# Performance work log

Hardware: AMD Instinct MI355X
Metric: run time of the kernel (lower is better)

## Reference

```python
import jax, jax.numpy as jnp
import numpy as np

V = 50000; C0 = 2000; C1 = 10000   # vocab and adaptive-softmax cutoffs
E = 512; H = 1024; B = 32; T = 128
H1 = H // 4; H2 = H // 16           # div_val = 4.0 per source formula
S1 = C1 - C0; S2 = V - C1


def setup_inputs() -> dict:
    key = jax.random.key(0)
    ks = jax.random.split(key, 12)
    # lengths sorted descending, max length == T (required by output.view(b*(T-1),-1))
    lengths = jnp.sort(jax.random.randint(ks[0], (B,), T // 2, T + 1))[::-1]
    lengths = lengths.at[0].set(T).astype(jnp.int64)
    x = jax.random.randint(ks[1], (B, T), 1, V)
    x = jnp.where(jnp.arange(T)[None, :] < lengths[:, None], x, 0).astype(jnp.int64)  # PAD=0 beyond length
    emb = (jax.random.normal(ks[2], (V, E), jnp.float32) * 0.02).at[0].set(0.0)  # padding_idx=0
    w_ih = jax.random.normal(ks[3], (3 * H, E), jnp.float32) * 0.02
    w_hh = jax.random.normal(ks[4], (3 * H, H), jnp.float32) * 0.02
    b_ih = jnp.zeros((3 * H,), jnp.float32)
    b_hh = jnp.zeros((3 * H,), jnp.float32)
    head_w = jax.random.normal(ks[5], (C0 + 2, H), jnp.float32) * 0.02   # shortlist + 2 cluster logits
    p1 = jax.random.normal(ks[6], (H1, H), jnp.float32) * 0.02
    t1 = jax.random.normal(ks[7], (S1, H1), jnp.float32) * 0.02
    p2 = jax.random.normal(ks[8], (H2, H), jnp.float32) * 0.02
    t2 = jax.random.normal(ks[9], (S2, H2), jnp.float32) * 0.02
    hidden = jnp.zeros((1, B, H), jnp.float32)
    return dict(x=x, lengths=lengths, hidden=hidden, emb=emb, w_ih=w_ih, w_hh=w_hh,
                b_ih=b_ih, b_hh=b_hh, head_w=head_w, p1=p1, t1=t1, p2=p2, t2=t2)


def gru_masked(inp, h0, w_ih, w_hh, b_ih, b_hh, lengths):
    """Torch GRU on packed sequence of lengths-1: frozen hidden + zero outputs past length."""
    xp = jnp.einsum('bte,ge->btg', inp, w_ih) + b_ih  # [B, T-1, 3H] input projections

    def step(h, args):
        xpt, t = args
        hp = h @ w_hh.T + b_hh
        xr, xz, xn = jnp.split(xpt, 3, axis=-1)
        hr, hz, hn = jnp.split(hp, 3, axis=-1)
        r = jax.nn.sigmoid(xr + hr)
        z = jax.nn.sigmoid(xz + hz)
        n = jnp.tanh(xn + r * hn)
        h_new = (1.0 - z) * n + z * h
        valid = (t < lengths - 1)[:, None]
        h = jnp.where(valid, h_new, h)          # freeze hidden past sequence end
        y = jnp.where(valid, h, 0.0)            # pad_packed_sequence zero-fills
        return h, y

    steps = jnp.arange(inp.shape[1])
    hT, ys = jax.lax.scan(step, h0, (jnp.swapaxes(xp, 0, 1), steps))
    return jnp.swapaxes(ys, 0, 1), hT  # [B, T-1, H], [B, H]


def adaptive_loss(out, targets, head_w, p1, t1, p2, t2):
    """AdaptiveLogSoftmaxWithLoss: mean NLL over shortlist + 2 tail clusters."""
    N = out.shape[0]
    head_lp = jax.nn.log_softmax(out @ head_w.T, axis=-1)  # [N, C0+2]
    idx = jnp.arange(N)
    lp_short = head_lp[idx, jnp.clip(targets, 0, C0 - 1)]

    def cluster_lp(p, t, ci, lo, size):
        tail_lp = jax.nn.log_softmax((out @ p.T) @ t.T, axis=-1)  # [N, size]
        rel = jnp.clip(targets - lo, 0, size - 1)
        return head_lp[:, C0 + ci] + tail_lp[idx, rel]

    lp1 = cluster_lp(p1, t1, 0, C0, S1)
    lp2 = cluster_lp(p2, t2, 1, C1, S2)
    logp = jnp.where(targets < C0, lp_short, jnp.where(targets < C1, lp1, lp2))
    return -jnp.mean(logp)


def reference(x, lengths, hidden, emb, w_ih, w_hh, b_ih, b_hh, head_w, p1, t1, p2, t2):
    inp = emb[x][:, :T - 1]  # dropout=0.0 -> identity
    ys, hT = gru_masked(inp, hidden[0], w_ih, w_hh, b_ih, b_hh, lengths)
    out = ys.reshape(B * (T - 1), H)
    targets = x[:, 1:].reshape(-1)
    loss = adaptive_loss(out, targets, head_w, p1, t1, p2, t2)
    return loss, hT[None]
```

## Files before the change

### kernel.cpp

```cpp
#include <hip/hip_runtime.h>
#include <math.h>

#define VV   50000
#define CC0  2000
#define CC1  10000
#define ED   512
#define HD   1024
#define BBATCH 32
#define TT   128
#define HH1  256
#define HH2  64
#define SS1  8000
#define SS2  40000
#define NR   4064
#define G3   3072

#define OFF_XP   0ull
#define OFF_YSB  12484608ull
#define OFF_HB   14565376ull
#define OFF_HT   14598144ull
#define OFF_P1B  14630912ull
#define OFF_P2B  15151104ull
#define OFF_WHB  15281152ull
#define OFF_T1B  16306176ull
#define OFF_PP1  17330176ull
#define OFF_PP2  17461248ull
#define OFF_SUM  17494016ull
#define OFF_LOSS (OFF_SUM + 6ull*4064ull)
#define OFF_INT  (OFF_LOSS + 64ull)
#define OFF_WIHB (OFF_INT + 8ull*4064ull)

#define ZERO_N (6*4064 + 64)
#define NBG 64

typedef __attribute__((ext_vector_type(8))) __bf16 bf16x8;
typedef __attribute__((ext_vector_type(4))) float f32x4;
typedef __attribute__((ext_vector_type(4))) unsigned int u32x4;
typedef unsigned long long u64;
typedef unsigned short u16;
struct ull2s { u64 x, y; };

__device__ __forceinline__ u16 f2bf(float f) {
    unsigned u = __builtin_bit_cast(unsigned, f);
    u += 0x7fff + ((u >> 16) & 1);
    return (u16)(u >> 16);
}

__global__ void init_k(const float* __restrict__ hidden, u16* __restrict__ hb0,
                       float* __restrict__ zreg, int* __restrict__ cnt1,
                       int* __restrict__ cnt2, int* __restrict__ bar)
{
    int i = blockIdx.x * 256 + threadIdx.x;
    if (i < BBATCH * HD) hb0[i] = f2bf(hidden[i]);
    int zi = i - BBATCH * HD;
    if (zi >= 0 && zi < ZERO_N) zreg[zi] = 0.f;
    if (zi == ZERO_N) { *cnt1 = 0; *cnt2 = 0; }
    int bi = zi - (ZERO_N + 1);
    if (bi >= 0 && bi < 2048) bar[bi] = 0;
}

__global__ void prep_k(const int* __restrict__ x, int* __restrict__ targets,
                       int* __restrict__ hselc, int* __restrict__ list1,
                       int* __restrict__ list2, int* __restrict__ cnt1, int* __restrict__ cnt2)
{
    int n = blockIdx.x * 256 + threadIdx.x;
    if (n >= NR) return;
    int b = n / 127, t = n % 127;
    int tgt = x[b * TT + t + 1];
    targets[n] = tgt;
    hselc[n] = (tgt < CC0) ? tgt : ((tgt < CC1) ? CC0 : CC0 + 1);
    if (tgt >= CC0 && tgt < CC1) list1[atomicAdd(cnt1, 1)] = n;
    else if (tgt >= CC1)         list2[atomicAdd(cnt2, 1)] = n;
}

__global__ void cvt_bf16_k(const float* __restrict__ src, u16* __restrict__ dst, int n4)
{
    int i = blockIdx.x * 256 + threadIdx.x;
    if (i >= n4) return;
    float4 f = *(const float4*)(src + 4 * (size_t)i);
    union { u16 h[4]; u64 v; } u;
    u.h[0] = f2bf(f.x); u.h[1] = f2bf(f.y); u.h[2] = f2bf(f.z); u.h[3] = f2bf(f.w);
    *(u64*)&dst[4 * (size_t)i] = u.v;
}

__global__ void cvt_multi_k(const float* __restrict__ s0, u16* __restrict__ d0, int n0,
                            const float* __restrict__ s1, u16* __restrict__ d1, int n1,
                            const float* __restrict__ s2, u16* __restrict__ d2, int n2,
                            const float* __restrict__ s3, u16* __restrict__ d3, int n3,
                            const float* __restrict__ s4, u16* __restrict__ d4, int n4)
{
    int i = blockIdx.x * 256 + threadIdx.x;
    const float* s; u16* d; int off = i;
    if (off < n0) { s = s0; d = d0; }
    else if ((off -= n0) < n1) { s = s1; d = d1; }
    else if ((off -= n1) < n2) { s = s2; d = d2; }
    else if ((off -= n2) < n3) { s = s3; d = d3; }
    else if ((off -= n3) < n4) { s = s4; d = d4; }
    else return;
    float4 f = *(const float4*)(s + 4 * (size_t)off);
    union { u16 h[4]; u64 v; } u;
    u.h[0] = f2bf(f.x); u.h[1] = f2bf(f.y); u.h[2] = f2bf(f.z); u.h[3] = f2bf(f.w);
    *(u64*)&d[4 * (size_t)off] = u.v;
}

__global__ void emb_gather_k(const int* __restrict__ x, const float* __restrict__ emb,
                             u16* __restrict__ embA)
{
    int idx = blockIdx.x * 256 + threadIdx.x;
    if (idx >= NR * 64) return;
    int n = idx >> 6;
    int kk = (idx & 63) << 3;
    int b = n & 31, t = n >> 5;
    int tok = x[b * TT + t];
    const float* ap = emb + (size_t)tok * ED + kk;
    float4 f0 = *(const float4*)ap;
    float4 f1 = *(const float4*)(ap + 4);
    union { u16 h[8]; u32x4 v; } u;
    u.h[0] = f2bf(f0.x); u.h[1] = f2bf(f0.y); u.h[2] = f2bf(f0.z); u.h[3] = f2bf(f0.w);
    u.h[4] = f2bf(f1.x); u.h[5] = f2bf(f1.y); u.h[6] = f2bf(f1.z); u.h[7] = f2bf(f1.w);
    *(u32x4*)&embA[(size_t)n * ED + kk] = u.v;
}

template<int EPI, int BFP32>
__global__ void __launch_bounds__(256)
mfma_gemm_k(const u16* __restrict__ Ab, const void* __restrict__ Bsrc,
            int Mdirect, int N, int K,
            const int* __restrict__ rowmap, const int* __restrict__ cntp,
            u16* __restrict__ outB, int ldo,
            float* __restrict__ gsum, float* __restrict__ gsel,
            const int* __restrict__ selcol, const int* __restrict__ targets, int lo)
{
    const int M = cntp ? *cntp : Mdirect;
    const int rbase = blockIdx.x * 128;
    if (rbase >= M) return;
    const int cbase = blockIdx.y * 128;

    __shared__ u16 As[128 * 40];
    __shared__ u16 Bs[128 * 40];
    __shared__ const u16* aptr[128];
    __shared__ int rown[128];
    __shared__ float redl[128 * 2];

    const int tid = threadIdx.x;
    if (tid < 128) {
        int rid = -1;
        if (rbase + tid < M) rid = rowmap ? rowmap[rbase + tid] : (rbase + tid);
        rown[tid] = rid;
        aptr[tid] = (rid >= 0) ? (Ab + (size_t)rid * K) : nullptr;
    }
    __syncthreads();

    const int lane = tid & 63, wid = tid >> 6;
    const int n16 = lane & 15, quad = lane >> 4;
    const int m0 = (wid >> 1) * 64, n0 = (wid & 1) * 64;
    const int i = tid >> 1, half = tid & 1;

    f32x4 acc[4][4];
#pragma unroll
    for (int a = 0; a < 4; a++)
#pragma unroll
        for (int b = 0; b < 4; b++) acc[a][b] = (f32x4){0.f, 0.f, 0.f, 0.f};

    for (int k0 = 0; k0 < K; k0 += 32) {
        const u16* ap = aptr[i];
        u32x4 a0 = {0,0,0,0}, a1 = a0;
        if (ap) {
            a0 = *(const u32x4*)(ap + k0 + half * 16);
            a1 = *(const u32x4*)(ap + k0 + half * 16 + 8);
        }
        u32x4 b0 = {0,0,0,0}, b1 = b0;
        int c = cbase + i;
        if (c < N) {
            if (BFP32) {
                const float* bp = (const float*)Bsrc + (size_t)c * K + k0 + half * 16;
                float4 f0 = *(const float4*)(bp);
                float4 f1 = *(const float4*)(bp + 4);
                float4 f2 = *(const float4*)(bp + 8);
                float4 f3 = *(const float4*)(bp + 12);
                union { u16 h[16]; u32x4 v[2]; } u;
                u.h[0]=f2bf(f0.x); u.h[1]=f2bf(f0.y); u.h[2]=f2bf(f0.z); u.h[3]=f2bf(f0.w);
                u.h[4]=f2bf(f1.x); u.h[5]=f2bf(f1.y); u.h[6]=f2bf(f1.z); u.h[7]=f2bf(f1.w);
                u.h[8]=f2bf(f2.x); u.h[9]=f2bf(f2.y); u.h[10]=f2bf(f2.z); u.h[11]=f2bf(f2.w);
                u.h[12]=f2bf(f3.x); u.h[13]=f2bf(f3.y); u.h[14]=f2bf(f3.z); u.h[15]=f2bf(f3.w);
                b0 = u.v[0]; b1 = u.v[1];
            } else {
                const u16* bp = (const u16*)Bsrc + (size_t)c * K + k0 + half * 16;
                b0 = *(const u32x4*)(bp);
                b1 = *(const u32x4*)(bp + 8);
            }
        }
        __syncthreads();
        *(u32x4*)&As[i * 40 + half * 16]     = a0;
        *(u32x4*)&As[i * 40 + half * 16 + 8] = a1;
        *(u32x4*)&Bs[i * 40 + half * 16]     = b0;
        *(u32x4*)&Bs[i * 40 + half * 16 + 8] = b1;
        __syncthreads();

        bf16x8 av[4], bv[4];
#pragma unroll
        for (int mi = 0; mi < 4; mi++)
            av[mi] = *(const bf16x8*)&As[(m0 + mi * 16 + n16) * 40 + quad * 8];
#pragma unroll
        for (int ni = 0; ni < 4; ni++)
            bv[ni] = *(const bf16x8*)&Bs[(n0 + ni * 16 + n16) * 40 + quad * 8];
#pragma unroll
        for (int mi = 0; mi < 4; mi++)
#pragma unroll
            for (int ni = 0; ni < 4; ni++)
                acc[mi][ni] = __builtin_amdgcn_mfma_f32_16x16x32_bf16(
                    av[mi], bv[ni], acc[mi][ni], 0, 0, 0);
    }

    __syncthreads();
    if (EPI == 0) {
#pragma unroll
        for (int mi = 0; mi < 4; mi++)
#pragma unroll
            for (int ni = 0; ni < 4; ni++)
#pragma unroll
                for (int r = 0; r < 4; r++) {
                    int row = rbase + m0 + mi * 16 + quad * 4 + r;
                    int col = cbase + n0 + ni * 16 + n16;
                    if (row < M && col < N)
                        outB[(size_t)row * ldo + col] = f2bf(acc[mi][ni][r]);
                }
    } else if (EPI == 3) {
#pragma unroll
        for (int mi = 0; mi < 4; mi++)
#pragma unroll
            for (int ni = 0; ni < 4; ni++)
#pragma unroll
                for (int r = 0; r < 4; r++) {
                    int row = rbase + m0 + mi * 16 + quad * 4 + r;
                    int col = cbase + n0 + ni * 16 + n16;
                    if (row < M && col < N)
                        gsum[(size_t)row * ldo + col] = acc[mi][ni][r] + gsel[col];
                }
    } else {
#pragma unroll
        for (int mi = 0; mi < 4; mi++)
#pragma unroll
            for (int r = 0; r < 4; r++) {
                int lrow = m0 + mi * 16 + quad * 4 + r;
                int nid = rown[lrow];
                float s = 0.f;
                if (nid >= 0) {
                    int sc = (EPI == 1) ? selcol[nid] : (targets[nid] - lo);
#pragma unroll
                    for (int ni = 0; ni < 4; ni++) {
                        int col = cbase + n0 + ni * 16 + n16;
                        if (col < N) {
                            float v = acc[mi][ni][r];
                            s += __expf(v);
                            if (col == sc) gsel[nid] = v;
                        }
                    }
                }
                s += __shfl_xor(s, 1);
                s += __shfl_xor(s, 2);
                s += __shfl_xor(s, 4);
                s += __shfl_xor(s, 8);
                if (n16 == 0) redl[lrow * 2 + (wid & 1)] = s;
            }
        __syncthreads();
        if (tid < 128) {
            int nid = rown[tid];
            if (nid >= 0) atomicAdd(&gsum[nid], redl[tid * 2] + redl[tid * 2 + 1]);
        }
    }
}

__global__ void __launch_bounds__(128, 1)
gru_persist_k(const float* __restrict__ xp, const float* __restrict__ hidden,
              u16* __restrict__ hb0, u16* __restrict__ hb1,
              const float* __restrict__ w_hh, const float* __restrict__ b_hh,
              const int* __restrict__ lengths, u16* __restrict__ ys,
              float* __restrict__ hT, int* __restrict__ cntbar)
{
    __shared__ u16 Blds[48 * 1032];
    const int tid = threadIdx.x;
    const int bid = blockIdx.x;
    const int j0 = bid * 16;
    const int lane = tid & 63, wid = tid >> 6;
    const int n16 = lane & 15, quad = lane >> 4;

    for (int idx = tid; idx < 48 * 1024; idx += 128) {
        int r = idx >> 10, k = idx & 1023;
        int g = r >> 4, c = r & 15;
        Blds[r * 1032 + k] = f2bf(w_hh[(size_t)(g * HD + j0 + c) * HD + k]);
    }

    const int col = j0 + n16;
    float bh0 = b_hh[col], bh1 = b_hh[HD + col], bh2 = b_hh[2 * HD + col];
    float hold[4];
    int len[4];
#pragma unroll
    for (int r = 0; r < 4; r++) {
        int b = wid * 16 + quad * 4 + r;
        len[r] = lengths[b];
        hold[r] = hidden[b * HD + col];
    }
    __syncthreads();

    float xrv[4], xzv[4], xnv[4];
#pragma unroll
    for (int r = 0; r < 4; r++) {
        int b = wid * 16 + quad * 4 + r;
        const float* xpt = xp + (size_t)b * G3 + col;
        xrv[r] = xpt[0]; xzv[r] = xpt[HD]; xnv[r] = xpt[2 * HD];
    }

    for (int t = 0; t < TT - 1; t++) {
        if (t > 0) {
            const int target = NBG * t;
            int guard = 0;
            while (__hip_atomic_load(cntbar, __ATOMIC_RELAXED,
                                     __HIP_MEMORY_SCOPE_AGENT) < target
                   && guard < (1 << 20)) {
                __builtin_amdgcn_s_sleep(1);
                guard++;
            }
        }
        asm volatile("" ::: "memory");

        const u16* hb = (t & 1) ? hb1 : hb0;
        u16* hbn = (t & 1) ? hb0 : hb1;

        const u16* arow = hb + (size_t)(wid * 16 + n16) * HD + quad * 8;
        u64 apf[64];
#pragma unroll
        for (int ks = 0; ks < 32; ks++) {
            apf[2*ks]   = __hip_atomic_load((const u64*)(arow + ks*32),
                                            __ATOMIC_RELAXED, __HIP_MEMORY_SCOPE_AGENT);
            apf[2*ks+1] = __hip_atomic_load((const u64*)(arow + ks*32 + 4),
                                            __ATOMIC_RELAXED, __HIP_MEMORY_SCOPE_AGENT);
        }

        f32x4 acc0 = {0.f, 0.f, 0.f, 0.f}, acc1 = acc0, acc2 = acc0;
        const int boff = n16 * 1032 + quad * 8;
#pragma unroll
        for (int ks = 0; ks < 32; ks++) {
            ull2s av2; av2.x = apf[2*ks]; av2.y = apf[2*ks+1];
            bf16x8 av = __builtin_bit_cast(bf16x8, av2);
            bf16x8 b0 = *(const bf16x8*)&Blds[boff + ks*32];
            bf16x8 b1 = *(const bf16x8*)&Blds[16*1032 + boff + ks*32];
            bf16x8 b2 = *(const bf16x8*)&Blds[32*1032 + boff + ks*32];
            acc0 = __builtin_amdgcn_mfma_f32_16x16x32_bf16(av, b0, acc0, 0, 0, 0);
            acc1 = __builtin_amdgcn_mfma_f32_16x16x32_bf16(av, b1, acc1, 0, 0, 0);
            acc2 = __builtin_amdgcn_mfma_f32_16x16x32_bf16(av, b2, acc2, 0, 0, 0);
        }

        float ysv[4];
#pragma unroll
        for (int r = 0; r < 4; r++) {
            int b = wid * 16 + quad * 4 + r;
            float hr = acc0[r] + bh0, hz = acc1[r] + bh1, hn = acc2[r] + bh2;
            float rg = 1.f / (1.f + __expf(-(xrv[r] + hr)));
            float zg = 1.f / (1.f + __expf(-(xzv[r] + hz)));
            float nv = tanhf(xnv[r] + rg * hn);
            bool valid = t < (len[r] - 1);
            float hnew = valid ? (1.f - zg) * nv + zg * hold[r] : hold[r];
            hold[r] = hnew;
            ysv[r] = valid ? hnew : 0.f;
            __hip_atomic_store(hbn + (size_t)b * HD + col, f2bf(hnew),
                               __ATOMIC_RELAXED, __HIP_MEMORY_SCOPE_AGENT);
        }

        __builtin_amdgcn_s_waitcnt(0);
        __syncthreads();
        if (tid == 0)
            __hip_atomic_fetch_add(cntbar, 1, __ATOMIC_RELAXED,
                                   __HIP_MEMORY_SCOPE_AGENT);

#pragma unroll
        for (int r = 0; r < 4; r++) {
            int b = wid * 16 + quad * 4 + r;
            ys[((size_t)b * 127 + t) * HD + col] = f2bf(ysv[r]);
            if (t == TT - 2) hT[b * HD + col] = hold[r];
        }
        const int tn = (t < TT - 2) ? t + 1 : t;
#pragma unroll
        for (int r = 0; r < 4; r++) {
            int b = wid * 16 + quad * 4 + r;
            const float* xpt = xp + ((size_t)tn * BBATCH + b) * G3 + col;
            xrv[r] = xpt[0]; xzv[r] = xpt[HD]; xnv[r] = xpt[2 * HD];
        }
    }
}

__global__ void finish_k(const float* __restrict__ hsum, const float* __restrict__ hsel,
                         const float* __restrict__ t1sum, const float* __restrict__ t1sel,
                         const float* __restrict__ t2sum, const float* __restrict__ t2sel,
                         const int* __restrict__ targets, float* __restrict__ losssum)
{
    __shared__ float red[256];
    int n = blockIdx.x * 256 + threadIdx.x;
    float lp = 0.f;
    if (n < NR) {
        lp = hsel[n] - logf(hsum[n]);
        int tgt = targets[n];
        if (tgt >= CC1)      lp += t2sel[n] - logf(t2sum[n]);
        else if (tgt >= CC0) lp += t1sel[n] - logf(t1sum[n]);
    }
    red[threadIdx.x] = lp;
    __syncthreads();
    for (int s = 128; s > 0; s >>= 1) {
        if (threadIdx.x < s) red[threadIdx.x] += red[threadIdx.x + s];
        __syncthreads();
    }
    if (threadIdx.x == 0) atomicAdd(losssum, red[0]);
}

__global__ void out_k(const float* __restrict__ losssum, const float* __restrict__ hT,
                      float* __restrict__ out)
{
    int i = blockIdx.x * 256 + threadIdx.x;
    if (i == 0) out[0] = -losssum[0] / (float)NR;
    if (i < BBATCH * HD) out[1 + i] = hT[i];
}

extern "C" void kernel_launch(void* const* d_in, const int* in_sizes, int n_in,
                              void* d_out, int out_size, void* d_ws, size_t ws_size,
                              hipStream_t stream)
{
    const int*   x       = (const int*)d_in[0];
    const int*   lengths = (const int*)d_in[1];
    const float* hidden  = (const float*)d_in[2];
    const float* emb     = (const float*)d_in[3];
    const float* w_ih    = (const float*)d_in[4];
    const float* w_hh    = (const float*)d_in[5];
    const float* b_ih    = (const float*)d_in[6];
    const float* b_hh    = (const float*)d_in[7];
    const float* head_w  = (const float*)d_in[8];
    const float* p1      = (const float*)d_in[9];
    const float* t1      = (const float*)d_in[10];
    const float* p2      = (const float*)d_in[11];
    const float* t2      = (const float*)d_in[12];

    float* ws = (float*)d_ws;
    float* xp    = ws + OFF_XP;
    u16*   ysb   = (u16*)(ws + OFF_YSB);
    u16*   hb0   = (u16*)(ws + OFF_HB);
    u16*   hb1   = hb0 + BBATCH * HD;
    float* hT    = ws + OFF_HT;
    u16*   p1b   = (u16*)(ws + OFF_P1B);
    u16*   p2b   = (u16*)(ws + OFF_P2B);
    u16*   whb   = (u16*)(ws + OFF_WHB);
    u16*   t1b   = (u16*)(ws + OFF_T1B);
    u16*   pp1b  = (u16*)(ws + OFF_PP1);
    u16*   pp2b  = (u16*)(ws + OFF_PP2);
    float* hsum  = ws + OFF_SUM;
    float* hsel  = hsum + 4064;
    float* t1sum = hsel + 4064;
    float* t1sel = t1sum + 4064;
    float* t2sum = t1sel + 4064;
    float* t2sel = t2sum + 4064;
    float* losss = ws + OFF_LOSS;
    int* ib      = (int*)(ws + OFF_INT);
    int* targets = ib;
    int* hselc   = ib + 4064;
    int* list1   = ib + 2 * 4064;
    int* list2   = ib + 3 * 4064;
    int* cnt1    = ib + 4 * 4064;
    int* cnt2    = cnt1 + 1;
    int* bar     = ib + 5 * 4064;

    u16* embA = (u16*)(ws + OFF_YSB);
    u16* wihb = (u16*)(ws + OFF_WIHB);
    u16* t2b  = (u16*)(ws + OFF_XP);

    float* out = (float*)d_out;

    init_k<<<232, 256, 0, stream>>>(hidden, hb0, hsum, cnt1, cnt2, bar);
    prep_k<<<16, 256, 0, stream>>>(x, targets, hselc, list1, list2, cnt1, cnt2);

    cvt_multi_k<<<(1499648 + 255) / 256, 256, 0, stream>>>(
        w_ih, wihb, 393216,
        head_w, whb, 512512,
        t1, t1b, 512000,
        p1, pp1b, 65536,
        p2, pp2b, 16384);

    emb_gather_k<<<(NR * 64 + 255) / 256, 256, 0, stream>>>(x, emb, embA);
    mfma_gemm_k<3, 0><<<dim3(32, 24), 256, 0, stream>>>(
        embA, wihb, NR, G3, ED, nullptr, nullptr, nullptr, G3,
        xp, (float*)b_ih, nullptr, nullptr, 0);

    gru_persist_k<<<NBG, 128, 0, stream>>>(xp, hidden, hb0, hb1, w_hh, b_hh,
                                           lengths, ysb, hT, bar);

    cvt_bf16_k<<<(640000 + 255) / 256, 256, 0, stream>>>(t2, t2b, 640000);

    mfma_gemm_k<0, 0><<<dim3(32, 2), 256, 0, stream>>>(
        ysb, pp1b, NR, HH1, HD, nullptr, nullptr, p1b, HH1,
        nullptr, nullptr, nullptr, nullptr, 0);
    mfma_gemm_k<0, 0><<<dim3(32, 1), 256, 0, stream>>>(
        ysb, pp2b, NR, HH2, HD, nullptr, nullptr, p2b, HH2,
        nullptr, nullptr, nullptr, nullptr, 0);
    mfma_gemm_k<1, 0><<<dim3(32, 16), 256, 0, stream>>>(
        ysb, whb, NR, CC0 + 2, HD, nullptr, nullptr, nullptr, 0,
        hsum, hsel, hselc, nullptr, 0);
    mfma_gemm_k<2, 0><<<dim3(32, 63), 256, 0, stream>>>(
        p1b, t1b, 0, SS1, HH1, list1, cnt1, nullptr, 0,
        t1sum, t1sel, nullptr, targets, CC0);
    mfma_gemm_k<2, 0><<<dim3(32, 313), 256, 0, stream>>>(
        p2b, t2b, 0, SS2, HH2, list2, cnt2, nullptr, 0,
        t2sum, t2sel, nullptr, targets, CC1);

    finish_k<<<16, 256, 0, stream>>>(hsum, hsel, t1sum, t1sel, t2sum, t2sel,
                                     targets, losss);
    out_k<<<128, 256, 0, stream>>>(losss, hT, out);
}
```

Measured before the change: 1.463 ms.

## Replace GRU grid counter barrier with per-block flags and triple-buffered hidden state

```diff
diff --git a/kernel.cpp b/kernel.cpp
--- a/kernel.cpp
+++ b/kernel.cpp
@@ -272,10 +272,10 @@
 
 __global__ void __launch_bounds__(128, 1)
 gru_persist_k(const float* __restrict__ xp, const float* __restrict__ hidden,
-              u16* __restrict__ hb0, u16* __restrict__ hb1,
+              u16* __restrict__ hb0, u16* __restrict__ hb1, u16* __restrict__ hb2,
               const float* __restrict__ w_hh, const float* __restrict__ b_hh,
               const int* __restrict__ lengths, u16* __restrict__ ys,
-              float* __restrict__ hT, int* __restrict__ cntbar)
+              float* __restrict__ hT, int* __restrict__ flags)
 {
     __shared__ u16 Blds[48 * 1032];
     const int tid = threadIdx.x;
@@ -310,44 +310,61 @@
         xrv[r] = xpt[0]; xzv[r] = xpt[HD]; xnv[r] = xpt[2 * HD];
     }
 
+    const int boff = n16 * 1032 + quad * 8;
+    const size_t rowoff = (size_t)(wid * 16 + n16) * HD + quad * 8;
+
     for (int t = 0; t < TT - 1; t++) {
-        if (t > 0) {
-            const int target = NBG * t;
-            int guard = 0;
-            while (__hip_atomic_load(cntbar, __ATOMIC_RELAXED,
-                                     __HIP_MEMORY_SCOPE_AGENT) < target
-                   && guard < (1 << 20)) {
-                __builtin_amdgcn_s_sleep(1);
-                guard++;
+        int m3 = t % 3;
+        const u16* hbR = (m3 == 0) ? hb0 : ((m3 == 1) ? hb1 : hb2);
+        int w3 = (t + 1) % 3;
+        u16* hbW = (w3 == 0) ? hb0 : ((w3 == 1) ? hb1 : hb2);
+
+        f32x4 acc0 = {0.f, 0.f, 0.f, 0.f}, acc1 = acc0, acc2 = acc0;
+
+        unsigned rem = 0xFFFFFFFFu;
+        int spin = 0;
+        while (rem) {
+            int f = __hip_atomic_load(&flags[lane * 32], __ATOMIC_RELAXED,
+                                      __HIP_MEMORY_SCOPE_AGENT);
+            u64 m = __ballot(f >= t);
+            u64 q = m & (m >> 1);
+            unsigned ready = 0;
+#pragma unroll
+            for (int ks = 0; ks < 32; ks++)
+                ready |= (unsigned)((q >> (2 * ks)) & 1ull) << ks;
+            unsigned todo = ready & rem;
+            if (!todo) {
+                if (++spin < (1 << 18)) { __builtin_amdgcn_s_sleep(2); continue; }
+                todo = rem;
             }
-        }
-        asm volatile("" ::: "memory");
-
-        const u16* hb = (t & 1) ? hb1 : hb0;
-        u16* hbn = (t & 1) ? hb0 : hb1;
-
-        const u16* arow = hb + (size_t)(wid * 16 + n16) * HD + quad * 8;
-        u64 apf[64];
-#pragma unroll
-        for (int ks = 0; ks < 32; ks++) {
-            apf[2*ks]   = __hip_atomic_load((const u64*)(arow + ks*32),
-                                            __ATOMIC_RELAXED, __HIP_MEMORY_SCOPE_AGENT);
-            apf[2*ks+1] = __hip_atomic_load((const u64*)(arow + ks*32 + 4),
-                                            __ATOMIC_RELAXED, __HIP_MEMORY_SCOPE_AGENT);
-        }
-
-        f32x4 acc0 = {0.f, 0.f, 0.f, 0.f}, acc1 = acc0, acc2 = acc0;
-        const int boff = n16 * 1032 + quad * 8;
-#pragma unroll
-        for (int ks = 0; ks < 32; ks++) {
-            ull2s av2; av2.x = apf[2*ks]; av2.y = apf[2*ks+1];
-            bf16x8 av = __builtin_bit_cast(bf16x8, av2);
-            bf16x8 b0 = *(const bf16x8*)&Blds[boff + ks*32];
-            bf16x8 b1 = *(const bf16x8*)&Blds[16*1032 + boff + ks*32];
-            bf16x8 b2 = *(const bf16x8*)&Blds[32*1032 + boff + ks*32];
-            acc0 = __builtin_amdgcn_mfma_f32_16x16x32_bf16(av, b0, acc0, 0, 0, 0);
-            acc1 = __builtin_amdgcn_mfma_f32_16x16x32_bf16(av, b1, acc1, 0, 0, 0);
-            acc2 = __builtin_amdgcn_mfma_f32_16x16x32_bf16(av, b2, acc2, 0, 0, 0);
+            todo = __builtin_amdgcn_readfirstlane(todo);
+            {
+                u64 a0buf[32], a1buf[32];
+#pragma unroll
+                for (int ks = 0; ks < 32; ks++) {
+                    if (todo & (1u << ks)) {
+                        const u16* ap = hbR + rowoff + ks * 32;
+                        a0buf[ks] = __hip_atomic_load((const u64*)ap,
+                                        __ATOMIC_RELAXED, __HIP_MEMORY_SCOPE_AGENT);
+                        a1buf[ks] = __hip_atomic_load((const u64*)(ap + 4),
+                                        __ATOMIC_RELAXED, __HIP_MEMORY_SCOPE_AGENT);
+                    }
+                }
+#pragma unroll
+                for (int ks = 0; ks < 32; ks++) {
+                    if (todo & (1u << ks)) {
+                        ull2s av2; av2.x = a0buf[ks]; av2.y = a1buf[ks];
+                        bf16x8 av = __builtin_bit_cast(bf16x8, av2);
+                        bf16x8 b0 = *(const bf16x8*)&Blds[boff + ks * 32];
+                        bf16x8 b1 = *(const bf16x8*)&Blds[16 * 1032 + boff + ks * 32];
+                        bf16x8 b2 = *(const bf16x8*)&Blds[32 * 1032 + boff + ks * 32];
+                        acc0 = __builtin_amdgcn_mfma_f32_16x16x32_bf16(av, b0, acc0, 0, 0, 0);
+                        acc1 = __builtin_amdgcn_mfma_f32_16x16x32_bf16(av, b1, acc1, 0, 0, 0);
+                        acc2 = __builtin_amdgcn_mfma_f32_16x16x32_bf16(av, b2, acc2, 0, 0, 0);
+                    }
+                }
+            }
+            rem &= ~todo;
         }
 
         float ysv[4];
@@ -362,15 +379,15 @@
             float hnew = valid ? (1.f - zg) * nv + zg * hold[r] : hold[r];
             hold[r] = hnew;
             ysv[r] = valid ? hnew : 0.f;
-            __hip_atomic_store(hbn + (size_t)b * HD + col, f2bf(hnew),
+            __hip_atomic_store(hbW + (size_t)b * HD + col, f2bf(hnew),
                                __ATOMIC_RELAXED, __HIP_MEMORY_SCOPE_AGENT);
         }
 
         __builtin_amdgcn_s_waitcnt(0);
         __syncthreads();
         if (tid == 0)
-            __hip_atomic_fetch_add(cntbar, 1, __ATOMIC_RELAXED,
-                                   __HIP_MEMORY_SCOPE_AGENT);
+            __hip_atomic_store(&flags[bid * 32], t + 1, __ATOMIC_RELAXED,
+                               __HIP_MEMORY_SCOPE_AGENT);
 
 #pragma unroll
         for (int r = 0; r < 4; r++) {
@@ -463,15 +480,16 @@
     int* list2   = ib + 3 * 4064;
     int* cnt1    = ib + 4 * 4064;
     int* cnt2    = cnt1 + 1;
-    int* bar     = ib + 5 * 4064;
+    int* flags   = ib + 5 * 4064;
 
     u16* embA = (u16*)(ws + OFF_YSB);
     u16* wihb = (u16*)(ws + OFF_WIHB);
     u16* t2b  = (u16*)(ws + OFF_XP);
+    u16* hb2  = (u16*)(ws + OFF_P1B);
 
     float* out = (float*)d_out;
 
-    init_k<<<232, 256, 0, stream>>>(hidden, hb0, hsum, cnt1, cnt2, bar);
+    init_k<<<232, 256, 0, stream>>>(hidden, hb0, hsum, cnt1, cnt2, flags);
     prep_k<<<16, 256, 0, stream>>>(x, targets, hselc, list1, list2, cnt1, cnt2);
 
     cvt_multi_k<<<(1499648 + 255) / 256, 256, 0, stream>>>(
@@ -486,8 +504,8 @@
         embA, wihb, NR, G3, ED, nullptr, nullptr, nullptr, G3,
         xp, (float*)b_ih, nullptr, nullptr, 0);
 
-    gru_persist_k<<<NBG, 128, 0, stream>>>(xp, hidden, hb0, hb1, w_hh, b_hh,
-                                           lengths, ysb, hT, bar);
+    gru_persist_k<<<NBG, 128, 0, stream>>>(xp, hidden, hb0, hb1, hb2, w_hh, b_hh,
+                                           lengths, ysb, hT, flags);
 
     cvt_bf16_k<<<(640000 + 255) / 256, 256, 0, stream>>>(t2, t2b, 640000);
 
```

Result: slower. 1.785 ms (+22.0%).

## Replace global counter barrier with per-block flags and partial early MFMA

Applied to the files above, without the earlier changes.

```diff
diff --git a/kernel.cpp b/kernel.cpp
--- a/kernel.cpp
+++ b/kernel.cpp
@@ -275,7 +275,7 @@
               u16* __restrict__ hb0, u16* __restrict__ hb1,
               const float* __restrict__ w_hh, const float* __restrict__ b_hh,
               const int* __restrict__ lengths, u16* __restrict__ ys,
-              float* __restrict__ hT, int* __restrict__ cntbar)
+              float* __restrict__ hT, int* __restrict__ flags)
 {
     __shared__ u16 Blds[48 * 1032];
     const int tid = threadIdx.x;
@@ -310,44 +310,107 @@
         xrv[r] = xpt[0]; xzv[r] = xpt[HD]; xnv[r] = xpt[2 * HD];
     }
 
+    const int boff = n16 * 1032 + quad * 8;
+    const size_t rowoff = (size_t)(wid * 16 + n16) * HD + quad * 8;
+
     for (int t = 0; t < TT - 1; t++) {
-        if (t > 0) {
-            const int target = NBG * t;
+        const u16* hbR = (t & 1) ? hb1 : hb0;
+        u16* hbW = (t & 1) ? hb0 : hb1;
+
+        f32x4 acc0 = {0.f, 0.f, 0.f, 0.f}, acc1 = acc0, acc2 = acc0;
+        u64 apf[64];
+
+        int fl = __hip_atomic_load(&flags[lane * 32], __ATOMIC_RELAXED,
+                                   __HIP_MEMORY_SCOPE_AGENT);
+        u64 rdy = __ballot(fl >= t);
+        unsigned done = 0;
+
+        if (rdy != ~0ull) {
+            u64 q = rdy & (rdy >> 1);
+            unsigned r0 = 0;
+#pragma unroll
+            for (int ks = 0; ks < 32; ks++)
+                r0 |= (unsigned)((q >> (2 * ks)) & 1ull) << ks;
+            r0 = __builtin_amdgcn_readfirstlane(r0);
+            asm volatile("" ::: "memory");
+            if (r0) {
+#pragma unroll
+                for (int ks = 0; ks < 32; ks++)
+                    if (r0 & (1u << ks)) {
+                        const u16* ap = hbR + rowoff + ks * 32;
+                        apf[2*ks]   = __hip_atomic_load((const u64*)ap,
+                                          __ATOMIC_RELAXED, __HIP_MEMORY_SCOPE_AGENT);
+                        apf[2*ks+1] = __hip_atomic_load((const u64*)(ap + 4),
+                                          __ATOMIC_RELAXED, __HIP_MEMORY_SCOPE_AGENT);
+                    }
+#pragma unroll
+                for (int ks = 0; ks < 32; ks++)
+                    if (r0 & (1u << ks)) {
+                        ull2s av2; av2.x = apf[2*ks]; av2.y = apf[2*ks+1];
+                        bf16x8 av = __builtin_bit_cast(bf16x8, av2);
+                        bf16x8 b0 = *(const bf16x8*)&Blds[boff + ks*32];
+                        bf16x8 b1 = *(const bf16x8*)&Blds[16*1032 + boff + ks*32];
+                        bf16x8 b2 = *(const bf16x8*)&Blds[32*1032 + boff + ks*32];
+                        acc0 = __builtin_amdgcn_mfma_f32_16x16x32_bf16(av, b0, acc0, 0, 0, 0);
+                        acc1 = __builtin_amdgcn_mfma_f32_16x16x32_bf16(av, b1, acc1, 0, 0, 0);
+                        acc2 = __builtin_amdgcn_mfma_f32_16x16x32_bf16(av, b2, acc2, 0, 0, 0);
+                    }
+                done = r0;
+            }
             int guard = 0;
-            while (__hip_atomic_load(cntbar, __ATOMIC_RELAXED,
-                                     __HIP_MEMORY_SCOPE_AGENT) < target
-                   && guard < (1 << 20)) {
+            while (true) {
+                fl = __hip_atomic_load(&flags[lane * 32], __ATOMIC_RELAXED,
+                                       __HIP_MEMORY_SCOPE_AGENT);
+                if (__ballot(fl >= t) == ~0ull) break;
+                if (++guard >= (1 << 20)) break;
                 __builtin_amdgcn_s_sleep(1);
-                guard++;
             }
         }
         asm volatile("" ::: "memory");
 
-        const u16* hb = (t & 1) ? hb1 : hb0;
-        u16* hbn = (t & 1) ? hb0 : hb1;
-
-        const u16* arow = hb + (size_t)(wid * 16 + n16) * HD + quad * 8;
-        u64 apf[64];
-#pragma unroll
-        for (int ks = 0; ks < 32; ks++) {
-            apf[2*ks]   = __hip_atomic_load((const u64*)(arow + ks*32),
-                                            __ATOMIC_RELAXED, __HIP_MEMORY_SCOPE_AGENT);
-            apf[2*ks+1] = __hip_atomic_load((const u64*)(arow + ks*32 + 4),
-                                            __ATOMIC_RELAXED, __HIP_MEMORY_SCOPE_AGENT);
-        }
-
-        f32x4 acc0 = {0.f, 0.f, 0.f, 0.f}, acc1 = acc0, acc2 = acc0;
-        const int boff = n16 * 1032 + quad * 8;
-#pragma unroll
-        for (int ks = 0; ks < 32; ks++) {
-            ull2s av2; av2.x = apf[2*ks]; av2.y = apf[2*ks+1];
-            bf16x8 av = __builtin_bit_cast(bf16x8, av2);
-            bf16x8 b0 = *(const bf16x8*)&Blds[boff + ks*32];
-            bf16x8 b1 = *(const bf16x8*)&Blds[16*1032 + boff + ks*32];
-            bf16x8 b2 = *(const bf16x8*)&Blds[32*1032 + boff + ks*32];
-            acc0 = __builtin_amdgcn_mfma_f32_16x16x32_bf16(av, b0, acc0, 0, 0, 0);
-            acc1 = __builtin_amdgcn_mfma_f32_16x16x32_bf16(av, b1, acc1, 0, 0, 0);
-            acc2 = __builtin_amdgcn_mfma_f32_16x16x32_bf16(av, b2, acc2, 0, 0, 0);
+        if (done == 0u) {
+#pragma unroll
+            for (int ks = 0; ks < 32; ks++) {
+                const u16* ap = hbR + rowoff + ks * 32;
+                apf[2*ks]   = __hip_atomic_load((const u64*)ap,
+                                  __ATOMIC_RELAXED, __HIP_MEMORY_SCOPE_AGENT);
+                apf[2*ks+1] = __hip_atomic_load((const u64*)(ap + 4),
+                                  __ATOMIC_RELAXED, __HIP_MEMORY_SCOPE_AGENT);
+            }
+#pragma unroll
+            for (int ks = 0; ks < 32; ks++) {
+                ull2s av2; av2.x = apf[2*ks]; av2.y = apf[2*ks+1];
+                bf16x8 av = __builtin_bit_cast(bf16x8, av2);
+                bf16x8 b0 = *(const bf16x8*)&Blds[boff + ks*32];
+                bf16x8 b1 = *(const bf16x8*)&Blds[16*1032 + boff + ks*32];
+                bf16x8 b2 = *(const bf16x8*)&Blds[32*1032 + boff + ks*32];
+                acc0 = __builtin_amdgcn_mfma_f32_16x16x32_bf16(av, b0, acc0, 0, 0, 0);
+                acc1 = __builtin_amdgcn_mfma_f32_16x16x32_bf16(av, b1, acc1, 0, 0, 0);
+                acc2 = __builtin_amdgcn_mfma_f32_16x16x32_bf16(av, b2, acc2, 0, 0, 0);
+            }
+        } else {
+            unsigned rem = ~done;
+#pragma unroll
+            for (int ks = 0; ks < 32; ks++)
+                if (rem & (1u << ks)) {
+                    const u16* ap = hbR + rowoff + ks * 32;
+                    apf[2*ks]   = __hip_atomic_load((const u64*)ap,
+                                      __ATOMIC_RELAXED, __HIP_MEMORY_SCOPE_AGENT);
+                    apf[2*ks+1] = __hip_atomic_load((const u64*)(ap + 4),
+                                      __ATOMIC_RELAXED, __HIP_MEMORY_SCOPE_AGENT);
+                }
+#pragma unroll
+            for (int ks = 0; ks < 32; ks++)
+                if (rem & (1u << ks)) {
+                    ull2s av2; av2.x = apf[2*ks]; av2.y = apf[2*ks+1];
+                    bf16x8 av = __builtin_bit_cast(bf16x8, av2);
+                    bf16x8 b0 = *(const bf16x8*)&Blds[boff + ks*32];
+                    bf16x8 b1 = *(const bf16x8*)&Blds[16*1032 + boff + ks*32];
+                    bf16x8 b2 = *(const bf16x8*)&Blds[32*1032 + boff + ks*32];
+                    acc0 = __builtin_amdgcn_mfma_f32_16x16x32_bf16(av, b0, acc0, 0, 0, 0);
+                    acc1 = __builtin_amdgcn_mfma_f32_16x16x32_bf16(av, b1, acc1, 0, 0, 0);
+                    acc2 = __builtin_amdgcn_mfma_f32_16x16x32_bf16(av, b2, acc2, 0, 0, 0);
+                }
         }
 
         float ysv[4];
@@ -362,15 +425,15 @@
             float hnew = valid ? (1.f - zg) * nv + zg * hold[r] : hold[r];
             hold[r] = hnew;
             ysv[r] = valid ? hnew : 0.f;
-            __hip_atomic_store(hbn + (size_t)b * HD + col, f2bf(hnew),
+            __hip_atomic_store(hbW + (size_t)b * HD + col, f2bf(hnew),
                                __ATOMIC_RELAXED, __HIP_MEMORY_SCOPE_AGENT);
         }
 
         __builtin_amdgcn_s_waitcnt(0);
         __syncthreads();
         if (tid == 0)
-            __hip_atomic_fetch_add(cntbar, 1, __ATOMIC_RELAXED,
-                                   __HIP_MEMORY_SCOPE_AGENT);
+            __hip_atomic_store(&flags[bid * 32], t + 1, __ATOMIC_RELAXED,
+                               __HIP_MEMORY_SCOPE_AGENT);
 
 #pragma unroll
         for (int r = 0; r < 4; r++) {
@@ -463,7 +526,7 @@
     int* list2   = ib + 3 * 4064;
     int* cnt1    = ib + 4 * 4064;
     int* cnt2    = cnt1 + 1;
-    int* bar     = ib + 5 * 4064;
+    int* flags   = ib + 5 * 4064;
 
     u16* embA = (u16*)(ws + OFF_YSB);
     u16* wihb = (u16*)(ws + OFF_WIHB);
@@ -471,7 +534,7 @@
 
     float* out = (float*)d_out;
 
-    init_k<<<232, 256, 0, stream>>>(hidden, hb0, hsum, cnt1, cnt2, bar);
+    init_k<<<232, 256, 0, stream>>>(hidden, hb0, hsum, cnt1, cnt2, flags);
     prep_k<<<16, 256, 0, stream>>>(x, targets, hselc, list1, list2, cnt1, cnt2);
 
     cvt_multi_k<<<(1499648 + 255) / 256, 256, 0, stream>>>(
@@ -487,7 +550,7 @@
         xp, (float*)b_ih, nullptr, nullptr, 0);
 
     gru_persist_k<<<NBG, 128, 0, stream>>>(xp, hidden, hb0, hb1, w_hh, b_hh,
-                                           lengths, ysb, hT, bar);
+                                           lengths, ysb, hT, flags);
 
     cvt_bf16_k<<<(640000 + 255) / 256, 256, 0, stream>>>(t2, t2b, 640000);
 
```

Measured after the change: 1.601 ms. 9.4% more time.

## Fuse GRU recurrence with head and projection GEMMs via per-timestep flags

Applied to the files above, without the earlier changes.

```diff
diff --git a/kernel.cpp b/kernel.cpp
--- a/kernel.cpp
+++ b/kernel.cpp
@@ -32,6 +32,8 @@
 
 #define ZERO_N (6*4064 + 64)
 #define NBG 64
+#define NCONS 192
+#define NTILES 608
 
 typedef __attribute__((ext_vector_type(8))) __bf16 bf16x8;
 typedef __attribute__((ext_vector_type(4))) float f32x4;
@@ -65,7 +67,7 @@
 {
     int n = blockIdx.x * 256 + threadIdx.x;
     if (n >= NR) return;
-    int b = n / 127, t = n % 127;
+    int t = n >> 5, b = n & 31;
     int tgt = x[b * TT + t + 1];
     targets[n] = tgt;
     hselc[n] = (tgt < CC0) ? tgt : ((tgt < CC1) ? CC0 : CC0 + 1);
@@ -270,120 +272,259 @@
     }
 }
 
-__global__ void __launch_bounds__(128, 1)
-gru_persist_k(const float* __restrict__ xp, const float* __restrict__ hidden,
-              u16* __restrict__ hb0, u16* __restrict__ hb1,
-              const float* __restrict__ w_hh, const float* __restrict__ b_hh,
-              const int* __restrict__ lengths, u16* __restrict__ ys,
-              float* __restrict__ hT, int* __restrict__ cntbar)
+__global__ void __launch_bounds__(256, 1)
+gru_fused_k(const float* __restrict__ xp, const float* __restrict__ hidden,
+            u16* __restrict__ hb0, u16* __restrict__ hb1,
+            const float* __restrict__ w_hh, const float* __restrict__ b_hh,
+            const int* __restrict__ lengths, u16* __restrict__ ys,
+            float* __restrict__ hT, int* __restrict__ flags,
+            const u16* __restrict__ whb, const u16* __restrict__ pp1b,
+            const u16* __restrict__ pp2b, u16* __restrict__ p1b,
+            u16* __restrict__ p2b, float* __restrict__ hsum,
+            float* __restrict__ hsel, const int* __restrict__ hselc)
 {
     __shared__ u16 Blds[48 * 1032];
+    __shared__ u16 As[128 * 40];
+    __shared__ u16 Bs[128 * 40];
+    __shared__ const u16* aptr[128];
+    __shared__ int rown[128];
+    __shared__ float redl[128 * 2];
+
     const int tid = threadIdx.x;
-    const int bid = blockIdx.x;
-    const int j0 = bid * 16;
-    const int lane = tid & 63, wid = tid >> 6;
+    const int lane = tid & 63;
     const int n16 = lane & 15, quad = lane >> 4;
 
-    for (int idx = tid; idx < 48 * 1024; idx += 128) {
-        int r = idx >> 10, k = idx & 1023;
-        int g = r >> 4, c = r & 15;
-        Blds[r * 1032 + k] = f2bf(w_hh[(size_t)(g * HD + j0 + c) * HD + k]);
-    }
-
-    const int col = j0 + n16;
-    float bh0 = b_hh[col], bh1 = b_hh[HD + col], bh2 = b_hh[2 * HD + col];
-    float hold[4];
-    int len[4];
-#pragma unroll
-    for (int r = 0; r < 4; r++) {
-        int b = wid * 16 + quad * 4 + r;
-        len[r] = lengths[b];
-        hold[r] = hidden[b * HD + col];
-    }
-    __syncthreads();
-
-    float xrv[4], xzv[4], xnv[4];
-#pragma unroll
-    for (int r = 0; r < 4; r++) {
-        int b = wid * 16 + quad * 4 + r;
-        const float* xpt = xp + (size_t)b * G3 + col;
-        xrv[r] = xpt[0]; xzv[r] = xpt[HD]; xnv[r] = xpt[2 * HD];
-    }
-
-    for (int t = 0; t < TT - 1; t++) {
-        if (t > 0) {
-            const int target = NBG * t;
-            int guard = 0;
-            while (__hip_atomic_load(cntbar, __ATOMIC_RELAXED,
-                                     __HIP_MEMORY_SCOPE_AGENT) < target
-                   && guard < (1 << 20)) {
-                __builtin_amdgcn_s_sleep(1);
-                guard++;
-            }
+    if (blockIdx.x < NBG) {
+        const int bid = blockIdx.x;
+        const int j0 = bid * 16;
+        const int wid = tid >> 6;
+
+        for (int idx = tid; idx < 48 * 1024; idx += 256) {
+            int r = idx >> 10, k = idx & 1023;
+            int g = r >> 4, c = r & 15;
+            Blds[r * 1032 + k] = f2bf(w_hh[(size_t)(g * HD + j0 + c) * HD + k]);
         }
-        asm volatile("" ::: "memory");
-
-        const u16* hb = (t & 1) ? hb1 : hb0;
-        u16* hbn = (t & 1) ? hb0 : hb1;
-
-        const u16* arow = hb + (size_t)(wid * 16 + n16) * HD + quad * 8;
-        u64 apf[64];
-#pragma unroll
-        for (int ks = 0; ks < 32; ks++) {
-            apf[2*ks]   = __hip_atomic_load((const u64*)(arow + ks*32),
-                                            __ATOMIC_RELAXED, __HIP_MEMORY_SCOPE_AGENT);
-            apf[2*ks+1] = __hip_atomic_load((const u64*)(arow + ks*32 + 4),
-                                            __ATOMIC_RELAXED, __HIP_MEMORY_SCOPE_AGENT);
+
+        const int col = j0 + n16;
+        float bh0 = 0.f, bh1 = 0.f, bh2 = 0.f;
+        float hold[4];
+        int len[4] = {0, 0, 0, 0};
+        if (tid < 128) {
+            bh0 = b_hh[col]; bh1 = b_hh[HD + col]; bh2 = b_hh[2 * HD + col];
+#pragma unroll
+            for (int r = 0; r < 4; r++) {
+                int b = wid * 16 + quad * 4 + r;
+                len[r] = lengths[b];
+                hold[r] = hidden[b * HD + col];
+            }
         }
-
-        f32x4 acc0 = {0.f, 0.f, 0.f, 0.f}, acc1 = acc0, acc2 = acc0;
+        __syncthreads();
+
         const int boff = n16 * 1032 + quad * 8;
-#pragma unroll
-        for (int ks = 0; ks < 32; ks++) {
-            ull2s av2; av2.x = apf[2*ks]; av2.y = apf[2*ks+1];
-            bf16x8 av = __builtin_bit_cast(bf16x8, av2);
-            bf16x8 b0 = *(const bf16x8*)&Blds[boff + ks*32];
-            bf16x8 b1 = *(const bf16x8*)&Blds[16*1032 + boff + ks*32];
-            bf16x8 b2 = *(const bf16x8*)&Blds[32*1032 + boff + ks*32];
-            acc0 = __builtin_amdgcn_mfma_f32_16x16x32_bf16(av, b0, acc0, 0, 0, 0);
-            acc1 = __builtin_amdgcn_mfma_f32_16x16x32_bf16(av, b1, acc1, 0, 0, 0);
-            acc2 = __builtin_amdgcn_mfma_f32_16x16x32_bf16(av, b2, acc2, 0, 0, 0);
+        const size_t rowoff = (size_t)(wid * 16 + n16) * HD + quad * 8;
+
+        for (int t = 0; t < TT - 1; t++) {
+            if (tid < 128) {
+                const u16* hb = (t & 1) ? hb1 : hb0;
+                u16* hbn = (t & 1) ? hb0 : hb1;
+
+                float xrv[4], xzv[4], xnv[4];
+#pragma unroll
+                for (int r = 0; r < 4; r++) {
+                    int b = wid * 16 + quad * 4 + r;
+                    const float* xpt = xp + ((size_t)t * BBATCH + b) * G3 + col;
+                    xrv[r] = xpt[0]; xzv[r] = xpt[HD]; xnv[r] = xpt[2 * HD];
+                }
+
+                const u16* arow = hb + rowoff;
+                u64 apf[64];
+#pragma unroll
+                for (int ks = 0; ks < 32; ks++) {
+                    apf[2*ks]   = __hip_atomic_load((const u64*)(arow + ks*32),
+                                      __ATOMIC_RELAXED, __HIP_MEMORY_SCOPE_AGENT);
+                    apf[2*ks+1] = __hip_atomic_load((const u64*)(arow + ks*32 + 4),
+                                      __ATOMIC_RELAXED, __HIP_MEMORY_SCOPE_AGENT);
+                }
+
+                f32x4 acc0 = {0.f, 0.f, 0.f, 0.f}, acc1 = acc0, acc2 = acc0;
+#pragma unroll
+                for (int ks = 0; ks < 32; ks++) {
+                    ull2s av2; av2.x = apf[2*ks]; av2.y = apf[2*ks+1];
+                    bf16x8 av = __builtin_bit_cast(bf16x8, av2);
+                    bf16x8 b0 = *(const bf16x8*)&Blds[boff + ks*32];
+                    bf16x8 b1 = *(const bf16x8*)&Blds[16*1032 + boff + ks*32];
+                    bf16x8 b2 = *(const bf16x8*)&Blds[32*1032 + boff + ks*32];
+                    acc0 = __builtin_amdgcn_mfma_f32_16x16x32_bf16(av, b0, acc0, 0, 0, 0);
+                    acc1 = __builtin_amdgcn_mfma_f32_16x16x32_bf16(av, b1, acc1, 0, 0, 0);
+                    acc2 = __builtin_amdgcn_mfma_f32_16x16x32_bf16(av, b2, acc2, 0, 0, 0);
+                }
+
+#pragma unroll
+                for (int r = 0; r < 4; r++) {
+                    int b = wid * 16 + quad * 4 + r;
+                    float hr = acc0[r] + bh0, hz = acc1[r] + bh1, hn = acc2[r] + bh2;
+                    float rg = 1.f / (1.f + __expf(-(xrv[r] + hr)));
+                    float zg = 1.f / (1.f + __expf(-(xzv[r] + hz)));
+                    float nv = tanhf(xnv[r] + rg * hn);
+                    bool valid = t < (len[r] - 1);
+                    float hnew = valid ? (1.f - zg) * nv + zg * hold[r] : hold[r];
+                    hold[r] = hnew;
+                    __hip_atomic_store(hbn + (size_t)b * HD + col, f2bf(hnew),
+                                       __ATOMIC_RELAXED, __HIP_MEMORY_SCOPE_AGENT);
+                    __hip_atomic_store(ys + ((size_t)t * BBATCH + b) * HD + col,
+                                       f2bf(valid ? hnew : 0.f),
+                                       __ATOMIC_RELAXED, __HIP_MEMORY_SCOPE_AGENT);
+                    if (t == TT - 2) hT[b * HD + col] = hnew;
+                }
+            }
+
+            __syncthreads();
+            if (tid < 64) {
+                if (tid == 0) {
+                    __builtin_amdgcn_s_waitcnt(0);
+                    __hip_atomic_store(&flags[bid * 32], t + 1, __ATOMIC_RELAXED,
+                                       __HIP_MEMORY_SCOPE_AGENT);
+                }
+                int guard = 0;
+                while (__hip_atomic_load(&flags[tid * 32], __ATOMIC_RELAXED,
+                                         __HIP_MEMORY_SCOPE_AGENT) < t + 1
+                       && guard < (1 << 20)) {
+                    __builtin_amdgcn_s_sleep(1);
+                    guard++;
+                }
+            }
+            asm volatile("" ::: "memory");
+            __syncthreads();
         }
-
-        float ysv[4];
-#pragma unroll
-        for (int r = 0; r < 4; r++) {
-            int b = wid * 16 + quad * 4 + r;
-            float hr = acc0[r] + bh0, hz = acc1[r] + bh1, hn = acc2[r] + bh2;
-            float rg = 1.f / (1.f + __expf(-(xrv[r] + hr)));
-            float zg = 1.f / (1.f + __expf(-(xzv[r] + hz)));
-            float nv = tanhf(xnv[r] + rg * hn);
-            bool valid = t < (len[r] - 1);
-            float hnew = valid ? (1.f - zg) * nv + zg * hold[r] : hold[r];
-            hold[r] = hnew;
-            ysv[r] = valid ? hnew : 0.f;
-            __hip_atomic_store(hbn + (size_t)b * HD + col, f2bf(hnew),
-                               __ATOMIC_RELAXED, __HIP_MEMORY_SCOPE_AGENT);
-        }
-
-        __builtin_amdgcn_s_waitcnt(0);
-        __syncthreads();
-        if (tid == 0)
-            __hip_atomic_fetch_add(cntbar, 1, __ATOMIC_RELAXED,
-                                   __HIP_MEMORY_SCOPE_AGENT);
-
-#pragma unroll
-        for (int r = 0; r < 4; r++) {
-            int b = wid * 16 + quad * 4 + r;
-            ys[((size_t)b * 127 + t) * HD + col] = f2bf(ysv[r]);
-            if (t == TT - 2) hT[b * HD + col] = hold[r];
-        }
-        const int tn = (t < TT - 2) ? t + 1 : t;
-#pragma unroll
-        for (int r = 0; r < 4; r++) {
-            int b = wid * 16 + quad * 4 + r;
-            const float* xpt = xp + ((size_t)tn * BBATCH + b) * G3 + col;
-            xrv[r] = xpt[0]; xzv[r] = xpt[HD]; xnv[r] = xpt[2 * HD];
+    } else {
+        const int wid4 = tid >> 6;
+        const int m0 = (wid4 >> 1) * 64, n0 = (wid4 & 1) * 64;
+        const int i = tid >> 1, half = tid & 1;
+        const int cb = blockIdx.x - NBG;
+
+        for (int g = cb; g < NTILES; g += NCONS) {
+            int x, y, N, ldo = 0, epi;
+            const u16* Bp; u16* outp = nullptr;
+            if (g < 512)      { x = g >> 4;  y = g & 15; N = CC0 + 2; Bp = whb;  epi = 1; }
+            else if (g < 576) { int gg = g - 512; x = gg >> 1; y = gg & 1;
+                                N = HH1; Bp = pp1b; outp = p1b; ldo = HH1; epi = 0; }
+            else              { x = g - 576; y = 0;
+                                N = HH2; Bp = pp2b; outp = p2b; ldo = HH2; epi = 0; }
+            const int rbase = x * 128, cbase = y * 128;
+
+            int tneed = 4 * x + 4; if (tneed > TT - 1) tneed = TT - 1;
+            {
+                int guard = 0;
+                while (true) {
+                    int f = __hip_atomic_load(&flags[lane * 32], __ATOMIC_RELAXED,
+                                              __HIP_MEMORY_SCOPE_AGENT);
+                    if (__ballot(f >= tneed) == ~0ull) break;
+                    if (++guard >= (1 << 20)) break;
+                    __builtin_amdgcn_s_sleep(8);
+                }
+            }
+            asm volatile("" ::: "memory");
+
+            __syncthreads();
+            if (tid < 128) {
+                int rid = (rbase + tid < NR) ? (rbase + tid) : -1;
+                rown[tid] = rid;
+                aptr[tid] = (rid >= 0) ? (ys + (size_t)rid * HD) : nullptr;
+            }
+            __syncthreads();
+
+            f32x4 acc[4][4];
+#pragma unroll
+            for (int a = 0; a < 4; a++)
+#pragma unroll
+                for (int b = 0; b < 4; b++) acc[a][b] = (f32x4){0.f, 0.f, 0.f, 0.f};
+
+            for (int k0 = 0; k0 < HD; k0 += 32) {
+                const u16* ap = aptr[i];
+                u64 a0 = 0, a1 = 0, a2 = 0, a3 = 0;
+                if (ap) {
+                    const u64* p = (const u64*)(ap + k0 + half * 16);
+                    a0 = __hip_atomic_load(p,     __ATOMIC_RELAXED, __HIP_MEMORY_SCOPE_AGENT);
+                    a1 = __hip_atomic_load(p + 1, __ATOMIC_RELAXED, __HIP_MEMORY_SCOPE_AGENT);
+                    a2 = __hip_atomic_load(p + 2, __ATOMIC_RELAXED, __HIP_MEMORY_SCOPE_AGENT);
+                    a3 = __hip_atomic_load(p + 3, __ATOMIC_RELAXED, __HIP_MEMORY_SCOPE_AGENT);
+                }
+                u32x4 b0v = {0,0,0,0}, b1v = b0v;
+                int c = cbase + i;
+                if (c < N) {
+                    const u16* bp = Bp + (size_t)c * HD + k0 + half * 16;
+                    b0v = *(const u32x4*)(bp);
+                    b1v = *(const u32x4*)(bp + 8);
+                }
+                __syncthreads();
+                *(u64*)&As[i * 40 + half * 16]      = a0;
+                *(u64*)&As[i * 40 + half * 16 + 4]  = a1;
+                *(u64*)&As[i * 40 + half * 16 + 8]  = a2;
+                *(u64*)&As[i * 40 + half * 16 + 12] = a3;
+                *(u32x4*)&Bs[i * 40 + half * 16]     = b0v;
+                *(u32x4*)&Bs[i * 40 + half * 16 + 8] = b1v;
+                __syncthreads();
+
+                bf16x8 av[4], bv[4];
+#pragma unroll
+                for (int mi = 0; mi < 4; mi++)
+                    av[mi] = *(const bf16x8*)&As[(m0 + mi * 16 + n16) * 40 + quad * 8];
+#pragma unroll
+                for (int ni = 0; ni < 4; ni++)
+                    bv[ni] = *(const bf16x8*)&Bs[(n0 + ni * 16 + n16) * 40 + quad * 8];
+#pragma unroll
+                for (int mi = 0; mi < 4; mi++)
+#pragma unroll
+                    for (int ni = 0; ni < 4; ni++)
+                        acc[mi][ni] = __builtin_amdgcn_mfma_f32_16x16x32_bf16(
+                            av[mi], bv[ni], acc[mi][ni], 0, 0, 0);
+            }
+
+            __syncthreads();
+            if (epi == 0) {
+#pragma unroll
+                for (int mi = 0; mi < 4; mi++)
+#pragma unroll
+                    for (int ni = 0; ni < 4; ni++)
+#pragma unroll
+                        for (int r = 0; r < 4; r++) {
+                            int row = rbase + m0 + mi * 16 + quad * 4 + r;
+                            int col = cbase + n0 + ni * 16 + n16;
+                            if (row < NR && col < N)
+                                outp[(size_t)row * ldo + col] = f2bf(acc[mi][ni][r]);
+                        }
+            } else {
+#pragma unroll
+                for (int mi = 0; mi < 4; mi++)
+#pragma unroll
+                    for (int r = 0; r < 4; r++) {
+                        int lrow = m0 + mi * 16 + quad * 4 + r;
+                        int nid = rown[lrow];
+                        float s = 0.f;
+                        if (nid >= 0) {
+                            int sc = hselc[nid];
+#pragma unroll
+                            for (int ni = 0; ni < 4; ni++) {
+                                int col = cbase + n0 + ni * 16 + n16;
+                                if (col < N) {
+                                    float v = acc[mi][ni][r];
+                                    s += __expf(v);
+                                    if (col == sc) hsel[nid] = v;
+                                }
+                            }
+                        }
+                        s += __shfl_xor(s, 1);
+                        s += __shfl_xor(s, 2);
+                        s += __shfl_xor(s, 4);
+                        s += __shfl_xor(s, 8);
+                        if (n16 == 0) redl[lrow * 2 + (wid4 & 1)] = s;
+                    }
+                __syncthreads();
+                if (tid < 128) {
+                    int nid = rown[tid];
+                    if (nid >= 0) atomicAdd(&hsum[nid], redl[tid * 2] + redl[tid * 2 + 1]);
+                }
+            }
         }
     }
 }
@@ -463,7 +604,7 @@
     int* list2   = ib + 3 * 4064;
     int* cnt1    = ib + 4 * 4064;
     int* cnt2    = cnt1 + 1;
-    int* bar     = ib + 5 * 4064;
+    int* flags   = ib + 5 * 4064;
 
     u16* embA = (u16*)(ws + OFF_YSB);
     u16* wihb = (u16*)(ws + OFF_WIHB);
@@ -471,7 +612,7 @@
 
     float* out = (float*)d_out;
 
-    init_k<<<232, 256, 0, stream>>>(hidden, hb0, hsum, cnt1, cnt2, bar);
+    init_k<<<232, 256, 0, stream>>>(hidden, hb0, hsum, cnt1, cnt2, flags);
     prep_k<<<16, 256, 0, stream>>>(x, targets, hselc, list1, list2, cnt1, cnt2);
 
     cvt_multi_k<<<(1499648 + 255) / 256, 256, 0, stream>>>(
@@ -486,20 +627,12 @@
         embA, wihb, NR, G3, ED, nullptr, nullptr, nullptr, G3,
         xp, (float*)b_ih, nullptr, nullptr, 0);
 
-    gru_persist_k<<<NBG, 128, 0, stream>>>(xp, hidden, hb0, hb1, w_hh, b_hh,
-                                           lengths, ysb, hT, bar);
+    gru_fused_k<<<NBG + NCONS, 256, 0, stream>>>(
+        xp, hidden, hb0, hb1, w_hh, b_hh, lengths, ysb, hT, flags,
+        whb, pp1b, pp2b, p1b, p2b, hsum, hsel, hselc);
 
     cvt_bf16_k<<<(640000 + 255) / 256, 256, 0, stream>>>(t2, t2b, 640000);
 
-    mfma_gemm_k<0, 0><<<dim3(32, 2), 256, 0, stream>>>(
-        ysb, pp1b, NR, HH1, HD, nullptr, nullptr, p1b, HH1,
-        nullptr, nullptr, nullptr, nullptr, 0);
-    mfma_gemm_k<0, 0><<<dim3(32, 1), 256, 0, stream>>>(
-        ysb, pp2b, NR, HH2, HD, nullptr, nullptr, p2b, HH2,
-        nullptr, nullptr, nullptr, nullptr, 0);
-    mfma_gemm_k<1, 0><<<dim3(32, 16), 256, 0, stream>>>(
-        ysb, whb, NR, CC0 + 2, HD, nullptr, nullptr, nullptr, 0,
-        hsum, hsel, hselc, nullptr, 0);
     mfma_gemm_k<2, 0><<<dim3(32, 63), 256, 0, stream>>>(
         p1b, t1b, 0, SS1, HH1, list1, cnt1, nullptr, 0,
         t1sum, t1sel, nullptr, targets, CC0);
```

Measured after the change: 1.354 ms. 7.5% less time.
